# Kernel optimization log

Hardware: AMD Instinct MI355X
Metric: run time of the kernel (lower is better)

Reference implementation:

```python
import jax, jax.numpy as jnp
import numpy as np

L, B, VOCAB, K, D, NUM_LAYERS = 256, 32, 30000, 620, 2400, 4


def setup_inputs() -> dict:
    key = jax.random.key(0)
    ks = jax.random.split(key, 10)
    inp = {
        "tokens": jax.random.randint(ks[0], (L, B), 0, VOCAB, dtype=jnp.int32),
        "emb": jax.random.normal(ks[1], (VOCAB, K), dtype=jnp.float32) * 0.1,
        # layer 0: n_in (K) != n_out (D) -> k=4 projections (z, f, r, highway transform)
        "W0": jax.random.normal(ks[2], (K, 4 * D), dtype=jnp.float32) * (1.0 / np.sqrt(K)),
        "b0": jnp.zeros((2 * D,), dtype=jnp.float32),
    }
    for i in range(1, NUM_LAYERS):
        inp[f"W{i}"] = jax.random.normal(ks[2 + i], (D, 3 * D), dtype=jnp.float32) * (1.0 / np.sqrt(D))
        inp[f"b{i}"] = jnp.zeros((2 * D,), dtype=jnp.float32)
    return inp


def _scan_cell(f, z):
    # c_t = f_t * c_{t-1} + (1 - f_t) * z_t ; c_0 = 0.  f, z: (L, B, D)
    def step(c, fz):
        f_t, z_t = fz
        c = f_t * c + (1.0 - f_t) * z_t
        return c, c
    c0 = jnp.zeros(f.shape[1:], f.dtype)
    _, cs = jax.lax.scan(step, c0, (f, z))
    return cs  # (L, B, D)


def _sru_layer(x, W, b):
    # x: (L, B, n_in); W: (n_in, k*D); b: (2*D,)
    k = W.shape[1] // D
    U = jnp.einsum('lbi,io->lbo', x, W).reshape(x.shape[0], x.shape[1], k, D)
    z = U[..., 0, :]
    f = jax.nn.sigmoid(U[..., 1, :] + b[:D])
    r = jax.nn.sigmoid(U[..., 2, :] + b[D:])
    c = _scan_cell(f, z)
    x_skip = U[..., 3, :] if k == 4 else x  # highway transform when dims differ
    h = r * jnp.tanh(c) + (1.0 - r) * x_skip
    return h


def reference(tokens, emb, W0, b0, W1, b1, W2, b2, W3, b3):
    x = emb[tokens]  # (L, B, K) embedding gather
    for W, b in ((W0, b0), (W1, b1), (W2, b2), (W3, b3)):
        x = _sru_layer(x, W, b)
    # L2-normalize over hidden dim
    out = x / jnp.linalg.norm(x, ord=2, axis=2, keepdims=True)
    return out
```

## Files before the change

kernel.cpp:

```cpp
#include <hip/hip_runtime.h>
#include <cstdint>
#include <cstddef>

typedef unsigned short u16;
typedef unsigned char u8;

constexpr int L_ = 256, B_ = 32, D_ = 2400;
constexpr int K0 = 620, K0P = 640;
constexpr int N0 = 9600;
constexpr int NL = 7200, NLP = 7296;
constexpr int KL = 2400, KLP = 2432;
constexpr int MR = L_ * B_;

constexpr size_t SZ_XBUF = (size_t)MR * KLP * 2;
constexpr size_t SZ_UB   = (size_t)MR * N0 * 2;
constexpr size_t OFF_XA  = 0;
constexpr size_t OFF_XB  = SZ_XBUF;
constexpr size_t OFF_U   = 2 * SZ_XBUF;
constexpr size_t WS_REQ  = OFF_U + SZ_UB;
constexpr size_t SZ_WT0  = (size_t)N0 * K0P * 2;
constexpr size_t OFF_WT0 = OFF_XA + SZ_XBUF - SZ_WT0;
static_assert(OFF_WT0 % 256 == 0, "");
constexpr size_t SZ_X0   = (size_t)MR * K0P * 2;
static_assert(SZ_X0 <= SZ_XBUF, "");
constexpr size_t WT_L_OFF = (size_t)MR * NLP * 2;
static_assert(WT_L_OFF + (size_t)NLP * KLP * 2 <= SZ_UB, "WtL must fit in U tail");

typedef __bf16 bf16x8 __attribute__((ext_vector_type(8)));
typedef float floatx4 __attribute__((ext_vector_type(4)));

__device__ __forceinline__ u16 f2bf(float x) {
  unsigned u = __float_as_uint(x);
  unsigned r = 0x7fffu + ((u >> 16) & 1u);
  return (u16)((u + r) >> 16);
}
__device__ __forceinline__ float bf2f(u16 v) {
  return __uint_as_float((unsigned)v << 16);
}
__device__ __forceinline__ float frcp(float x) { return __builtin_amdgcn_rcpf(x); }
__device__ __forceinline__ float fsigmoid(float x) { return frcp(1.f + __expf(-x)); }
__device__ __forceinline__ float ftanh(float x) {
  return 1.f - 2.f * frcp(__expf(2.f * x) + 1.f);
}

__device__ __forceinline__ void gload_lds16(const void* g, void* l) {
  __builtin_amdgcn_global_load_lds(
      (__attribute__((address_space(1))) void*)g,
      (__attribute__((address_space(3))) void*)l,
      16, 0, 0);
}

__global__ void probe_fill(float* __restrict__ out, int n, float v) {
  int i = blockIdx.x * blockDim.x + threadIdx.x;
  if (i < n) out[i] = v;
}

__global__ void transpose_bf16_kernel(const float* __restrict__ W, u16* __restrict__ Wt,
                                      int K, int N, int Kpad, int Nrows) {
  __shared__ float tile[32][33];
  int kb = blockIdx.x * 32, nb = blockIdx.y * 32;
  int tx = threadIdx.x & 31, ty = threadIdx.x >> 5;
  #pragma unroll
  for (int i = ty; i < 32; i += 8) {
    int k = kb + i, n = nb + tx;
    tile[i][tx] = (k < K && n < N) ? W[(size_t)k * N + n] : 0.f;
  }
  __syncthreads();
  #pragma unroll
  for (int i = ty; i < 32; i += 8) {
    int n = nb + i, k = kb + tx;
    if (n < Nrows && k < Kpad)
      Wt[(size_t)n * Kpad + k] = f2bf(tile[tx][i]);
  }
}

__global__ void embed_kernel(const int* __restrict__ tokens, const float* __restrict__ emb,
                             u16* __restrict__ xbf) {
  int t = blockIdx.x;
  int tok = tokens[t];
  const float* src = emb + (size_t)tok * K0;
  u16* dst = xbf + (size_t)t * K0P;
  for (int k = threadIdx.x; k < K0P; k += blockDim.x)
    dst[k] = (k < K0) ? f2bf(src[k]) : (u16)0;
}

__global__ void zero_pad_x(u16* __restrict__ x) {
  int r = blockIdx.x * blockDim.x + threadIdx.x;
  if (r >= MR) return;
  uint4* p = (uint4*)(x + (size_t)r * KLP + KL);
  p[0] = make_uint4(0, 0, 0, 0);
  p[1] = make_uint4(0, 0, 0, 0);
  p[2] = make_uint4(0, 0, 0, 0);
  p[3] = make_uint4(0, 0, 0, 0);
}

__global__ __launch_bounds__(256, 4)
void gemm_nt_bf16(const u16* __restrict__ A, const u16* __restrict__ Bt,
                  u16* __restrict__ C, int M, int N, int K) {
  __shared__ __align__(16) u16 As[128 * 64];
  __shared__ __align__(16) u16 Bs[128 * 64];
  const int tid  = threadIdx.x;
  const int lane = tid & 63;
  const int wave = tid >> 6;
  const int wr   = (wave >> 1) * 64;
  const int wc   = (wave & 1) * 64;
  const int quad = lane >> 4;
  const int l16  = lane & 15;
  const size_t m0 = (size_t)blockIdx.x * 128;
  const size_t n0 = (size_t)blockIdx.y * 128;

  const int srow   = tid >> 3;
  const int gchunk = (tid & 7) ^ (srow & 7);
  const u16* aSrc = A + (m0 + srow) * (size_t)K + gchunk * 8;
  const u16* bSrc = Bt + (n0 + srow) * (size_t)K + gchunk * 8;
  const size_t rowStep = (size_t)32 * K;

  char* ldsA = (char*)As + wave * 1024;
  char* ldsB = (char*)Bs + wave * 1024;

  const int sw   = l16 & 7;
  const int off0 = ((quad    ) ^ sw) * 16;
  const int off1 = ((quad + 4) ^ sw) * 16;

  floatx4 acc[4][4] = {};

  for (int k0 = 0; k0 < K; k0 += 64) {
    #pragma unroll
    for (int i = 0; i < 4; ++i)
      gload_lds16(aSrc + (size_t)i * rowStep, ldsA + i * 4096);
    #pragma unroll
    for (int i = 0; i < 4; ++i)
      gload_lds16(bSrc + (size_t)i * rowStep, ldsB + i * 4096);
    aSrc += 64; bSrc += 64;
    __syncthreads();
    {
      bf16x8 af[4], bfr[4];
      #pragma unroll
      for (int i = 0; i < 4; ++i)
        af[i] = *(const bf16x8*)((const char*)As + (wr + i * 16 + l16) * 128 + off0);
      #pragma unroll
      for (int j = 0; j < 4; ++j)
        bfr[j] = *(const bf16x8*)((const char*)Bs + (wc + j * 16 + l16) * 128 + off0);
      #pragma unroll
      for (int i = 0; i < 4; ++i)
        #pragma unroll
        for (int j = 0; j < 4; ++j)
          acc[i][j] = __builtin_amdgcn_mfma_f32_16x16x32_bf16(af[i], bfr[j], acc[i][j], 0, 0, 0);
    }
    {
      bf16x8 af[4], bfr[4];
      #pragma unroll
      for (int i = 0; i < 4; ++i)
        af[i] = *(const bf16x8*)((const char*)As + (wr + i * 16 + l16) * 128 + off1);
      #pragma unroll
      for (int j = 0; j < 4; ++j)
        bfr[j] = *(const bf16x8*)((const char*)Bs + (wc + j * 16 + l16) * 128 + off1);
      #pragma unroll
      for (int i = 0; i < 4; ++i)
        #pragma unroll
        for (int j = 0; j < 4; ++j)
          acc[i][j] = __builtin_amdgcn_mfma_f32_16x16x32_bf16(af[i], bfr[j], acc[i][j], 0, 0, 0);
    }
    __syncthreads();
  }

  #pragma unroll
  for (int i = 0; i < 4; ++i) {
    size_t row = m0 + wr + i * 16 + quad * 4;
    #pragma unroll
    for (int j = 0; j < 4; ++j) {
      size_t col = n0 + wc + j * 16 + l16;
      u16* cp = C + row * (size_t)N + col;
      #pragma unroll
      for (int r = 0; r < 4; ++r)
        cp[(size_t)r * N] = f2bf(acc[i][j][r]);
    }
  }
}

__global__ __launch_bounds__(256, 2)
void sru_scan_kernel(const u16* __restrict__ U, int SN,
                     const float* __restrict__ bias,
                     const u16* skip, int skipStride,
                     u16* hbf, float* h32) {
  __shared__ float A_l[8 * 32];
  __shared__ float C_l[8 * 32];
  const int tid = threadIdx.x;
  const int j  = tid >> 5;
  const int dd = tid & 31;
  const int b  = blockIdx.x / (D_ / 32);
  const int d  = (blockIdx.x % (D_ / 32)) * 32 + dd;
  const float bfb = bias[d], brb = bias[D_ + d];
  const size_t rstep = (size_t)B_ * SN;
  const size_t sstep = (size_t)B_ * skipStride;
  const size_t hstep = (size_t)B_ * KLP;
  const size_t fstep = (size_t)B_ * D_;
  const u16* Up = U + (size_t)(j * 32) * rstep + (size_t)b * SN + d;
  const u16* Sp = skip + (size_t)(j * 32) * sstep + (size_t)b * skipStride + d;

  float cl[32], P[32];
  {
    float c = 0.f, A = 1.f;
    #pragma unroll
    for (int l = 0; l < 32; ++l) {
      float z  = bf2f(Up[l * rstep]);
      float fr = bf2f(Up[l * rstep + D_]);
      float f = fsigmoid(fr + bfb);
      c = f * c + (1.f - f) * z;
      A *= f;
      cl[l] = c; P[l] = A;
    }
    A_l[tid] = A;
    C_l[tid] = c;
  }
  __syncthreads();
  float Cin = 0.f;
  #pragma unroll
  for (int jj = 0; jj < 7; ++jj) {
    float a  = A_l[jj * 32 + dd];
    float cc = C_l[jj * 32 + dd];
    if (jj < j) Cin = a * Cin + cc;
  }

  u16*   hb = hbf ? hbf + (size_t)(j * 32) * hstep + (size_t)b * KLP + d : nullptr;
  float* hf = h32 ? h32 + (size_t)(j * 32) * fstep + (size_t)b * D_ + d : nullptr;
  #pragma unroll
  for (int l = 0; l < 32; ++l) {
    float rr = bf2f(Up[l * rstep + 2 * D_]);
    float xs = bf2f(Sp[l * sstep]);
    float r = fsigmoid(rr + brb);
    float cf = cl[l] + P[l] * Cin;
    float h = r * ftanh(cf) + (1.f - r) * xs;
    if (hb) hb[l * hstep] = f2bf(h);
    if (hf) hf[l * fstep] = h;
  }
}

__global__ void normalize_kernel(float* __restrict__ x) {
  __shared__ float red[4];
  int row = blockIdx.x;
  float* p = x + (size_t)row * D_;
  float s = 0.f;
  for (int d = threadIdx.x; d < D_; d += 256) { float v = p[d]; s += v * v; }
  #pragma unroll
  for (int o = 32; o > 0; o >>= 1) s += __shfl_down(s, o, 64);
  int lane = threadIdx.x & 63, w = threadIdx.x >> 6;
  if (lane == 0) red[w] = s;
  __syncthreads();
  if (threadIdx.x == 0) red[0] = 1.f / sqrtf(red[0] + red[1] + red[2] + red[3]);
  __syncthreads();
  float inv = red[0];
  for (int d = threadIdx.x; d < D_; d += 256) p[d] *= inv;
}

extern "C" void kernel_launch(void* const* d_in, const int* in_sizes, int n_in,
                              void* d_out, int out_size, void* d_ws, size_t ws_size,
                              hipStream_t stream) {
  const int*   tokens = (const int*)d_in[0];
  const float* emb = (const float*)d_in[1];
  const float* W0 = (const float*)d_in[2];
  const float* b0 = (const float*)d_in[3];
  const float* W1 = (const float*)d_in[4];
  const float* b1 = (const float*)d_in[5];
  const float* W2 = (const float*)d_in[6];
  const float* b2 = (const float*)d_in[7];
  const float* W3 = (const float*)d_in[8];
  const float* b3 = (const float*)d_in[9];
  float* out = (float*)d_out;

  if (ws_size < WS_REQ) {
    probe_fill<<<(out_size + 255) / 256, 256, 0, stream>>>(out, out_size,
                                                           (float)(ws_size >> 20));
    return;
  }

  char* ws = (char*)d_ws;
  u16* xa  = (u16*)(ws + OFF_XA);
  u16* xb  = (u16*)(ws + OFF_XB);
  u16* Ub  = (u16*)(ws + OFF_U);
  u16* Wt0 = (u16*)(ws + OFF_WT0);
  u16* x0  = xb;
  u16* WtL = (u16*)((char*)Ub + WT_L_OFF);

  dim3 blk(256);
  const int scanGrid = B_ * (D_ / 32);
  const int padGrid = (MR + 255) / 256;

  embed_kernel<<<MR, 256, 0, stream>>>(tokens, emb, x0);
  transpose_bf16_kernel<<<dim3(K0P / 32, N0 / 32), blk, 0, stream>>>(W0, Wt0, K0, N0, K0P, N0);
  gemm_nt_bf16<<<dim3(MR / 128, N0 / 128), blk, 0, stream>>>(x0, Wt0, Ub, MR, N0, K0P);
  zero_pad_x<<<padGrid, 256, 0, stream>>>(xa);
  zero_pad_x<<<padGrid, 256, 0, stream>>>(xb);
  sru_scan_kernel<<<scanGrid, 256, 0, stream>>>(Ub, N0, b0, Ub + 3 * D_, N0, xa, nullptr);

  transpose_bf16_kernel<<<dim3(KLP / 32, NLP / 32), blk, 0, stream>>>(W1, WtL, KL, NL, KLP, NLP);
  gemm_nt_bf16<<<dim3(MR / 128, NLP / 128), blk, 0, stream>>>(xa, WtL, Ub, MR, NLP, KLP);
  sru_scan_kernel<<<scanGrid, 256, 0, stream>>>(Ub, NLP, b1, xa, KLP, xb, nullptr);

  transpose_bf16_kernel<<<dim3(KLP / 32, NLP / 32), blk, 0, stream>>>(W2, WtL, KL, NL, KLP, NLP);
  gemm_nt_bf16<<<dim3(MR / 128, NLP / 128), blk, 0, stream>>>(xb, WtL, Ub, MR, NLP, KLP);
  sru_scan_kernel<<<scanGrid, 256, 0, stream>>>(Ub, NLP, b2, xb, KLP, xa, nullptr);

  transpose_bf16_kernel<<<dim3(KLP / 32, NLP / 32), blk, 0, stream>>>(W3, WtL, KL, NL, KLP, NLP);
  gemm_nt_bf16<<<dim3(MR / 128, NLP / 128), blk, 0, stream>>>(xa, WtL, Ub, MR, NLP, KLP);
  sru_scan_kernel<<<scanGrid, 256, 0, stream>>>(Ub, NLP, b3, xa, KLP, nullptr, out);

  normalize_kernel<<<MR, 256, 0, stream>>>(out);
}
```

Measured before the change: 1.561 ms.

## Replace 128x128 GEMM with double-buffered 256x256 tile kernel with staged prefetch

Replaces the 128x128 single-buffered bf16 MFMA GEMM with a 512-thread, 256x256-tile kernel that double-buffers LDS and interleaves global-to-LDS prefetch of the next K tiles across four MFMA phases. Raw s_barrier, explicit waitcnt, and setprio keep the MFMAs and loads overlapped. Workgroup index swizzling groups neighbouring tiles for cache locality. N padding grows to multiples of 256, which adds some wasted compute and memory, and the larger tile means fewer workgroups, which can leave CUs underused.

```diff
diff --git a/kernel.cpp b/kernel.cpp
--- a/kernel.cpp
+++ b/kernel.cpp
@@ -7,18 +7,18 @@
 
 constexpr int L_ = 256, B_ = 32, D_ = 2400;
 constexpr int K0 = 620, K0P = 640;
-constexpr int N0 = 9600;
-constexpr int NL = 7200, NLP = 7296;
+constexpr int N0 = 9600, N0P = 9728;
+constexpr int NL = 7200, NLP = 7424;
 constexpr int KL = 2400, KLP = 2432;
 constexpr int MR = L_ * B_;
 
 constexpr size_t SZ_XBUF = (size_t)MR * KLP * 2;
-constexpr size_t SZ_UB   = (size_t)MR * N0 * 2;
+constexpr size_t SZ_UB   = (size_t)MR * N0P * 2;
 constexpr size_t OFF_XA  = 0;
 constexpr size_t OFF_XB  = SZ_XBUF;
 constexpr size_t OFF_U   = 2 * SZ_XBUF;
 constexpr size_t WS_REQ  = OFF_U + SZ_UB;
-constexpr size_t SZ_WT0  = (size_t)N0 * K0P * 2;
+constexpr size_t SZ_WT0  = (size_t)N0P * K0P * 2;
 constexpr size_t OFF_WT0 = OFF_XA + SZ_XBUF - SZ_WT0;
 static_assert(OFF_WT0 % 256 == 0, "");
 constexpr size_t SZ_X0   = (size_t)MR * K0P * 2;
@@ -94,82 +94,128 @@
   p[3] = make_uint4(0, 0, 0, 0);
 }
 
-__global__ __launch_bounds__(256, 4)
-void gemm_nt_bf16(const u16* __restrict__ A, const u16* __restrict__ Bt,
-                  u16* __restrict__ C, int M, int N, int K) {
-  __shared__ __align__(16) u16 As[128 * 64];
-  __shared__ __align__(16) u16 Bs[128 * 64];
+#define FRAG_A(i, OFF) (*(const bf16x8*)(pa + (wrl + (i) * 16 + l16) * 128 + (OFF)))
+#define FRAG_B(j, OFF) (*(const bf16x8*)(pb + (wcl + (j) * 16 + l16) * 128 + (OFF)))
+
+#define MFMA_Q(Q)                                                                      \
+  _Pragma("unroll")                                                                    \
+  for (int j = 0; j < 4; ++j) {                                                        \
+    acc[2*(Q)][j]   = __builtin_amdgcn_mfma_f32_16x16x32_bf16(a0, bq[j][0], acc[2*(Q)][j],   0, 0, 0); \
+    acc[2*(Q)][j]   = __builtin_amdgcn_mfma_f32_16x16x32_bf16(a1, bq[j][1], acc[2*(Q)][j],   0, 0, 0); \
+    acc[2*(Q)+1][j] = __builtin_amdgcn_mfma_f32_16x16x32_bf16(a2, bq[j][0], acc[2*(Q)+1][j], 0, 0, 0); \
+    acc[2*(Q)+1][j] = __builtin_amdgcn_mfma_f32_16x16x32_bf16(a3, bq[j][1], acc[2*(Q)+1][j], 0, 0, 0); \
+  }
+
+#define PHASE_TAIL(Q)                                                                  \
+  __builtin_amdgcn_s_barrier();                                                        \
+  asm volatile("s_waitcnt lgkmcnt(0)" ::: "memory");                                   \
+  __builtin_amdgcn_sched_barrier(0);                                                   \
+  __builtin_amdgcn_s_setprio(1);                                                       \
+  MFMA_Q(Q);                                                                           \
+  __builtin_amdgcn_s_setprio(0);                                                       \
+  __builtin_amdgcn_s_barrier();
+
+__global__ __launch_bounds__(512, 2)
+void gemm_nt_bf16_256(const u16* __restrict__ A, const u16* __restrict__ Bt,
+                      u16* __restrict__ C, int M, int N, int K) {
+  __shared__ __align__(16) u16 As[2][256 * 64];
+  __shared__ __align__(16) u16 Bs[2][256 * 64];
   const int tid  = threadIdx.x;
   const int lane = tid & 63;
   const int wave = tid >> 6;
-  const int wr   = (wave >> 1) * 64;
-  const int wc   = (wave & 1) * 64;
   const int quad = lane >> 4;
   const int l16  = lane & 15;
-  const size_t m0 = (size_t)blockIdx.x * 128;
-  const size_t n0 = (size_t)blockIdx.y * 128;
-
-  const int srow   = tid >> 3;
-  const int gchunk = (tid & 7) ^ (srow & 7);
-  const u16* aSrc = A + (m0 + srow) * (size_t)K + gchunk * 8;
-  const u16* bSrc = Bt + (n0 + srow) * (size_t)K + gchunk * 8;
-  const size_t rowStep = (size_t)32 * K;
-
-  char* ldsA = (char*)As + wave * 1024;
-  char* ldsB = (char*)Bs + wave * 1024;
-
   const int sw   = l16 & 7;
-  const int off0 = ((quad    ) ^ sw) * 16;
-  const int off1 = ((quad + 4) ^ sw) * 16;
-
-  floatx4 acc[4][4] = {};
-
-  for (int k0 = 0; k0 < K; k0 += 64) {
-    #pragma unroll
-    for (int i = 0; i < 4; ++i)
-      gload_lds16(aSrc + (size_t)i * rowStep, ldsA + i * 4096);
-    #pragma unroll
-    for (int i = 0; i < 4; ++i)
-      gload_lds16(bSrc + (size_t)i * rowStep, ldsB + i * 4096);
-    aSrc += 64; bSrc += 64;
-    __syncthreads();
+  const int wrl  = (wave >> 2) * 128;
+  const int wcl  = (wave & 3) * 64;
+
+  const int nwg = gridDim.x * gridDim.y;
+  const int lin = blockIdx.y * gridDim.x + blockIdx.x;
+  const int swz = ((nwg & 7) == 0) ? ((lin & 7) * (nwg >> 3) + (lin >> 3)) : lin;
+  const int bx = swz % gridDim.x;
+  const int by = swz / gridDim.x;
+  const size_t m0 = (size_t)bx * 256;
+  const size_t n0 = (size_t)by * 256;
+
+  const int NT = K >> 6;
+
+  const int srow = tid >> 3;
+  const int gch  = (tid & 7) ^ (srow & 7);
+  const u16* aS = A  + (m0 + srow) * (size_t)K + gch * 8;
+  const u16* bS = Bt + (n0 + srow) * (size_t)K + gch * 8;
+  const size_t blkStep = (size_t)64 * K;
+  const int ldsOff = wave * 1024;
+
+  auto stgA = [&](int buf, int ib, int kt) {
+    gload_lds16(aS + (size_t)kt * 64 + (size_t)ib * blkStep,
+                (char*)As[buf] + ib * 8192 + ldsOff);
+  };
+  auto stgB = [&](int buf, int ib, int kt) {
+    gload_lds16(bS + (size_t)kt * 64 + (size_t)ib * blkStep,
+                (char*)Bs[buf] + ib * 8192 + ldsOff);
+  };
+
+  const int offk0 = (quad ^ sw) * 16;
+  const int offk1 = ((quad + 4) ^ sw) * 16;
+
+  floatx4 acc[8][4] = {};
+
+  #pragma unroll
+  for (int ib = 0; ib < 4; ++ib) stgA(0, ib, 0);
+  #pragma unroll
+  for (int ib = 0; ib < 4; ++ib) stgB(0, ib, 0);
+  #pragma unroll
+  for (int ib = 0; ib < 4; ++ib) stgB(1, ib, 1);
+  stgA(1, 0, 1);
+  stgA(1, 2, 1);
+  asm volatile("s_waitcnt vmcnt(6)" ::: "memory");
+  __builtin_amdgcn_s_barrier();
+
+  for (int t = 0; t < NT; ++t) {
+    const int buf = t & 1;
+    const char* pa = (const char*)As[buf];
+    const char* pb = (const char*)Bs[buf];
+    bf16x8 bq[4][2];
+
     {
-      bf16x8 af[4], bfr[4];
+      bf16x8 a0 = FRAG_A(0, offk0), a1 = FRAG_A(0, offk1);
+      bf16x8 a2 = FRAG_A(1, offk0), a3 = FRAG_A(1, offk1);
       #pragma unroll
-      for (int i = 0; i < 4; ++i)
-        af[i] = *(const bf16x8*)((const char*)As + (wr + i * 16 + l16) * 128 + off0);
-      #pragma unroll
-      for (int j = 0; j < 4; ++j)
-        bfr[j] = *(const bf16x8*)((const char*)Bs + (wc + j * 16 + l16) * 128 + off0);
-      #pragma unroll
-      for (int i = 0; i < 4; ++i)
-        #pragma unroll
-        for (int j = 0; j < 4; ++j)
-          acc[i][j] = __builtin_amdgcn_mfma_f32_16x16x32_bf16(af[i], bfr[j], acc[i][j], 0, 0, 0);
+      for (int j = 0; j < 4; ++j) {
+        bq[j][0] = FRAG_B(j, offk0);
+        bq[j][1] = FRAG_B(j, offk1);
+      }
+      if (t + 1 < NT) { stgA(buf ^ 1, 1, t + 1); stgA(buf ^ 1, 3, t + 1); }
+      PHASE_TAIL(0);
     }
     {
-      bf16x8 af[4], bfr[4];
-      #pragma unroll
-      for (int i = 0; i < 4; ++i)
-        af[i] = *(const bf16x8*)((const char*)As + (wr + i * 16 + l16) * 128 + off1);
-      #pragma unroll
-      for (int j = 0; j < 4; ++j)
-        bfr[j] = *(const bf16x8*)((const char*)Bs + (wc + j * 16 + l16) * 128 + off1);
-      #pragma unroll
-      for (int i = 0; i < 4; ++i)
-        #pragma unroll
-        for (int j = 0; j < 4; ++j)
-          acc[i][j] = __builtin_amdgcn_mfma_f32_16x16x32_bf16(af[i], bfr[j], acc[i][j], 0, 0, 0);
-    }
-    __syncthreads();
-  }
-
-  #pragma unroll
-  for (int i = 0; i < 4; ++i) {
-    size_t row = m0 + wr + i * 16 + quad * 4;
+      bf16x8 a0 = FRAG_A(2, offk0), a1 = FRAG_A(2, offk1);
+      bf16x8 a2 = FRAG_A(3, offk0), a3 = FRAG_A(3, offk1);
+      if (t + 2 < NT) { stgB(buf, 0, t + 2); stgB(buf, 1, t + 2); }
+      PHASE_TAIL(1);
+    }
+    {
+      bf16x8 a0 = FRAG_A(4, offk0), a1 = FRAG_A(4, offk1);
+      bf16x8 a2 = FRAG_A(5, offk0), a3 = FRAG_A(5, offk1);
+      if (t + 2 < NT) { stgB(buf, 2, t + 2); stgB(buf, 3, t + 2); }
+      PHASE_TAIL(2);
+    }
+    {
+      bf16x8 a0 = FRAG_A(6, offk0), a1 = FRAG_A(6, offk1);
+      bf16x8 a2 = FRAG_A(7, offk0), a3 = FRAG_A(7, offk1);
+      if (t + 2 < NT) { stgA(buf, 0, t + 2); stgA(buf, 2, t + 2); }
+      if (t + 2 < NT)      asm volatile("s_waitcnt vmcnt(6)" ::: "memory");
+      else if (t + 1 < NT) asm volatile("s_waitcnt vmcnt(0)" ::: "memory");
+      PHASE_TAIL(3);
+    }
+  }
+
+  #pragma unroll
+  for (int i = 0; i < 8; ++i) {
+    size_t row = m0 + wrl + i * 16 + quad * 4;
     #pragma unroll
     for (int j = 0; j < 4; ++j) {
-      size_t col = n0 + wc + j * 16 + l16;
+      size_t col = n0 + wcl + j * 16 + l16;
       u16* cp = C + row * (size_t)N + col;
       #pragma unroll
       for (int r = 0; r < 4; ++r)
@@ -287,22 +333,22 @@
   const int padGrid = (MR + 255) / 256;
 
   embed_kernel<<<MR, 256, 0, stream>>>(tokens, emb, x0);
-  transpose_bf16_kernel<<<dim3(K0P / 32, N0 / 32), blk, 0, stream>>>(W0, Wt0, K0, N0, K0P, N0);
-  gemm_nt_bf16<<<dim3(MR / 128, N0 / 128), blk, 0, stream>>>(x0, Wt0, Ub, MR, N0, K0P);
+  transpose_bf16_kernel<<<dim3(K0P / 32, N0P / 32), blk, 0, stream>>>(W0, Wt0, K0, N0, K0P, N0P);
+  gemm_nt_bf16_256<<<dim3(MR / 256, N0P / 256), 512, 0, stream>>>(x0, Wt0, Ub, MR, N0P, K0P);
   zero_pad_x<<<padGrid, 256, 0, stream>>>(xa);
   zero_pad_x<<<padGrid, 256, 0, stream>>>(xb);
-  sru_scan_kernel<<<scanGrid, 256, 0, stream>>>(Ub, N0, b0, Ub + 3 * D_, N0, xa, nullptr);
+  sru_scan_kernel<<<scanGrid, 256, 0, stream>>>(Ub, N0P, b0, Ub + 3 * D_, N0P, xa, nullptr);
 
   transpose_bf16_kernel<<<dim3(KLP / 32, NLP / 32), blk, 0, stream>>>(W1, WtL, KL, NL, KLP, NLP);
-  gemm_nt_bf16<<<dim3(MR / 128, NLP / 128), blk, 0, stream>>>(xa, WtL, Ub, MR, NLP, KLP);
+  gemm_nt_bf16_256<<<dim3(MR / 256, NLP / 256), 512, 0, stream>>>(xa, WtL, Ub, MR, NLP, KLP);
   sru_scan_kernel<<<scanGrid, 256, 0, stream>>>(Ub, NLP, b1, xa, KLP, xb, nullptr);
 
   transpose_bf16_kernel<<<dim3(KLP / 32, NLP / 32), blk, 0, stream>>>(W2, WtL, KL, NL, KLP, NLP);
-  gemm_nt_bf16<<<dim3(MR / 128, NLP / 128), blk, 0, stream>>>(xb, WtL, Ub, MR, NLP, KLP);
+  gemm_nt_bf16_256<<<dim3(MR / 256, NLP / 256), 512, 0, stream>>>(xb, WtL, Ub, MR, NLP, KLP);
   sru_scan_kernel<<<scanGrid, 256, 0, stream>>>(Ub, NLP, b2, xb, KLP, xa, nullptr);
 
   transpose_bf16_kernel<<<dim3(KLP / 32, NLP / 32), blk, 0, stream>>>(W3, WtL, KL, NL, KLP, NLP);
-  gemm_nt_bf16<<<dim3(MR / 128, NLP / 128), blk, 0, stream>>>(xa, WtL, Ub, MR, NLP, KLP);
+  gemm_nt_bf16_256<<<dim3(MR / 256, NLP / 256), 512, 0, stream>>>(xa, WtL, Ub, MR, NLP, KLP);
   sru_scan_kernel<<<scanGrid, 256, 0, stream>>>(Ub, NLP, b3, xa, KLP, nullptr, out);
 
   normalize_kernel<<<MR, 256, 0, stream>>>(out);
```

After: 1.646 ms. 5.4% more time.
